# Kernel optimization log

Measured on AMD Instinct MI355X. Metric: run time of the kernel, lower is better.

## Reference

```python
import jax, jax.numpy as jnp
import numpy as np

L = 880      # flattened RootMLP param count: (1*8+8) + (8*96+96)
HID = 8      # MLP hidden width
OUT = 96     # 2*data_size
DS = 48      # data_size
T = 64       # sequence length
BATCH = 4


def setup_inputs() -> dict:
    key = jax.random.key(0)
    k1, k2, k3, k4, k5 = jax.random.split(key, 5)
    xs = jax.random.normal(k1, (BATCH, T, DS), jnp.float32)
    ts = jax.random.uniform(k2, (BATCH, T), dtype=jnp.float32)
    theta0 = 0.1 * jax.random.normal(k3, (L,), jnp.float32)
    # near-identity A so matrix powers up to A^(T-1) stay bounded
    A = 0.99 * jnp.eye(L, dtype=jnp.float32) + (0.01 / np.sqrt(L)) * jax.random.normal(k4, (L, L), jnp.float32)
    B = 0.01 * jax.random.normal(k5, (L, DS), jnp.float32)
    return {"xs": xs, "ts": ts, "theta0": theta0, "A": A, "B": B, "aux": 0}


def _forward(xs, ts, theta0, A, B):
    Bt, T_, _ = xs.shape
    I = jnp.eye(L, dtype=A.dtype)

    # A_pows[t] = A^t for t = 0..T-1, via a cumulative matmul scan
    def step(P, _):
        return P @ A, P
    _, pows = jax.lax.scan(step, I, None, length=T_)  # (T, L, L)

    # K_conv = [B, A^0(A-I)B, ..., A^(T-3)(A-I)B]  -> (T-1, L, DS)
    M = (A - I) @ B
    K_tail = jnp.einsum('tij,jd->tid', pows[:T_ - 2], M)
    K_conv = jnp.concatenate([B[None], K_tail], axis=0)

    # FFT circular convolution of input signal with K_conv over time
    u = xs[:, 1:, :]                      # (B, T-1, DS)
    u_f = jnp.fft.fft(u, axis=1)
    K_f = jnp.fft.fft(K_conv, axis=0)     # (T-1, L, DS)
    thetas = jnp.fft.ifft(jnp.einsum('tld,btd->btl', K_f, u_f), axis=1).real

    # initial-condition convolution with K_conv0 = A^tau, tau = 0..T-2
    K0 = pows[:T_ - 1]                    # (T-1, L, L)
    sig = jnp.zeros((Bt, T_ - 1, L), xs.dtype)
    sig = sig.at[:, 0, :].set(theta0)
    sig = sig.at[:, 1, :].set(-(xs[:, 0, :] @ B.T))
    sig_f = jnp.fft.fft(sig, axis=1)
    K0_f = jnp.fft.fft(K0, axis=0)
    phi0 = jnp.fft.ifft(jnp.einsum('tlm,btm->btl', K0_f, sig_f), axis=1).real

    thetas = thetas + phi0
    thetas = jnp.concatenate([jnp.broadcast_to(theta0, (Bt, 1, L)), thetas], axis=1)  # (B, T, L)

    # apply RootMLP (1 -> HID -> OUT) with params unflattened from thetas
    W0 = thetas[..., :HID]                                    # (B,T,HID): W0 is (HID,1)
    b0 = thetas[..., HID:2 * HID]
    W1 = thetas[..., 2 * HID:2 * HID + OUT * HID].reshape(Bt, T_, OUT, HID)
    b1 = thetas[..., 2 * HID + OUT * HID:]
    h = jax.nn.relu(W0 * ts[..., None] + b0)                  # (B,T,HID)
    out = jnp.einsum('btoh,bth->bto', W1, h) + b1             # (B,T,OUT)
    # reconstruction head: tanh means, softplus stds
    return jnp.concatenate([jnp.tanh(out[..., :DS]), jax.nn.softplus(out[..., DS:])], axis=-1)


def reference(xs, ts, theta0, A, B, aux):
    return _forward(xs, ts, theta0, A, B)
```

## Files before the change

### kernel.cpp

```cpp
#include <hip/hip_runtime.h>
#include <math.h>

typedef unsigned int uint;
typedef unsigned short ushort;
typedef short s16x8 __attribute__((ext_vector_type(8)));
typedef float f32x4 __attribute__((ext_vector_type(4)));
typedef uint u32x4 __attribute__((ext_vector_type(4)));

#define L     880
#define LP    896
#define NC    64
#define WSZ   (NC * LP)
#define DS    48
#define OUTD  96
#define KCV   3072
#define NZ    6

#define OFF_E    0
#define OFF_KDT  0
#define OFF_WF   4415488
#define OFF_WB   (OFF_WF + 63 * WSZ)
#define OFF_U    (OFF_WB + 63 * WSZ / 2)
#define OFF_PART (OFF_U + 256 * KCV / 2)

__device__ inline ushort f2b(float f) {
  uint u = __builtin_bit_cast(uint, f);
  u += 0x7fffu + ((u >> 16) & 1u);
  return (ushort)(u >> 16);
}
__device__ inline float b2f(ushort b) {
  uint u = ((uint)b) << 16;
  return __builtin_bit_cast(float, u);
}

__device__ __forceinline__ void gemm64(const ushort* __restrict__ Ag,
                                       const ushort* __restrict__ Bg,
                                       int Kdim, int kIters, int kOff, int m0, int n0,
                                       int tid, ushort (*As)[72], ushort (*Bs)[72],
                                       f32x4 acc[2][2]) {
  const int r = tid >> 2, kq = (tid & 3) * 16;
  const ushort* aptr = Ag + (size_t)(m0 + r) * Kdim + kOff + kq;
  const ushort* bptr = Bg + (size_t)(n0 + r) * Kdim + kOff + kq;
  const int wv = tid >> 6, lane = tid & 63;
  const int wm = (wv >> 1) * 32, wn = (wv & 1) * 32;
  const int lr = lane & 15, lg = lane >> 4;
  acc[0][0] = f32x4{0.f, 0.f, 0.f, 0.f};
  acc[0][1] = f32x4{0.f, 0.f, 0.f, 0.f};
  acc[1][0] = f32x4{0.f, 0.f, 0.f, 0.f};
  acc[1][1] = f32x4{0.f, 0.f, 0.f, 0.f};
  u32x4 ra0 = *(const u32x4*)aptr;
  u32x4 ra1 = *(const u32x4*)(aptr + 8);
  u32x4 rb0 = *(const u32x4*)bptr;
  u32x4 rb1 = *(const u32x4*)(bptr + 8);
  __syncthreads();
  *(u32x4*)&As[r][kq]     = ra0;
  *(u32x4*)&As[r][kq + 8] = ra1;
  *(u32x4*)&Bs[r][kq]     = rb0;
  *(u32x4*)&Bs[r][kq + 8] = rb1;
  if (kIters > 1) {
    ra0 = *(const u32x4*)(aptr + 64);
    ra1 = *(const u32x4*)(aptr + 72);
    rb0 = *(const u32x4*)(bptr + 64);
    rb1 = *(const u32x4*)(bptr + 72);
  }
  __syncthreads();
  for (int it = 0; it < kIters; ++it) {
    const int cur = (it & 1) * 64, nxt = cur ^ 64;
    s16x8 fa0[2], fa1[2], fb0[2], fb1[2];
#pragma unroll
    for (int k2 = 0; k2 < 2; ++k2) {
      fa0[k2] = *(const s16x8*)&As[cur + wm + lr][k2 * 32 + lg * 8];
      fa1[k2] = *(const s16x8*)&As[cur + wm + 16 + lr][k2 * 32 + lg * 8];
      fb0[k2] = *(const s16x8*)&Bs[cur + wn + lr][k2 * 32 + lg * 8];
      fb1[k2] = *(const s16x8*)&Bs[cur + wn + 16 + lr][k2 * 32 + lg * 8];
    }
    if (it + 1 < kIters) {
      *(u32x4*)&As[nxt + r][kq]     = ra0;
      *(u32x4*)&As[nxt + r][kq + 8] = ra1;
      *(u32x4*)&Bs[nxt + r][kq]     = rb0;
      *(u32x4*)&Bs[nxt + r][kq + 8] = rb1;
      if (it + 2 < kIters) {
        ra0 = *(const u32x4*)(aptr + (it + 2) * 64);
        ra1 = *(const u32x4*)(aptr + (it + 2) * 64 + 8);
        rb0 = *(const u32x4*)(bptr + (it + 2) * 64);
        rb1 = *(const u32x4*)(bptr + (it + 2) * 64 + 8);
      }
    }
#pragma unroll
    for (int k2 = 0; k2 < 2; ++k2) {
      acc[0][0] = __builtin_amdgcn_mfma_f32_16x16x32_bf16(fa0[k2], fb0[k2], acc[0][0], 0, 0, 0);
      acc[0][1] = __builtin_amdgcn_mfma_f32_16x16x32_bf16(fa0[k2], fb1[k2], acc[0][1], 0, 0, 0);
      acc[1][0] = __builtin_amdgcn_mfma_f32_16x16x32_bf16(fa1[k2], fb0[k2], acc[1][0], 0, 0, 0);
      acc[1][1] = __builtin_amdgcn_mfma_f32_16x16x32_bf16(fa1[k2], fb1[k2], acc[1][1], 0, 0, 0);
    }
    __syncthreads();
  }
}

__device__ __forceinline__ void kd_body(const float* __restrict__ WF, ushort* __restrict__ KDT,
                                        int j, int l0, int tid, float (*D)[65]) {
  __syncthreads();
  if (j < 63) {
    const float* Wj = WF + (size_t)j * WSZ;
    for (int e = tid; e < 48 * 64; e += 256) {
      int d = e >> 6, ll = e & 63;
      float v = Wj[d * LP + l0 + ll];
      if (j > 0) v -= Wj[-(int)WSZ + d * LP + l0 + ll];
      D[d][ll] = v;
    }
  } else {
    for (int e = tid; e < 48 * 64; e += 256) { int d = e >> 6, ll = e & 63; D[d][ll] = 0.f; }
  }
  __syncthreads();
  for (int e = tid; e < 48 * 64; e += 256) {
    int ll = e / 48, d = e - ll * 48;
    KDT[(size_t)(l0 + ll) * KCV + j * 48 + d] = f2b(D[d][ll]);
  }
}

__global__ __launch_bounds__(256) void k_prep(const float* __restrict__ A,
                                              const float* __restrict__ B,
                                              const float* __restrict__ th0,
                                              const float* __restrict__ xs,
                                              ushort* __restrict__ EN,
                                              ushort* __restrict__ ET,
                                              float* __restrict__ WF,
                                              ushort* __restrict__ WB,
                                              ushort* __restrict__ U) {
  const int blk = blockIdx.x;
  const int tid = threadIdx.x;
  if (blk < 196) {
    __shared__ float T[64][65];
    const int bi = (blk / 14) * 64, bj = (blk % 14) * 64;
    const int r = tid >> 2, c0 = (tid & 3) * 16;
    const int gi = bi + r;
#pragma unroll
    for (int q = 0; q < 4; ++q) {
      int c = c0 + q * 4, gj = bj + c;
      float4 v = {0.f, 0.f, 0.f, 0.f};
      if (gi < L && gj + 3 < L) {
        v = *(const float4*)(A + (size_t)gi * L + gj);
      } else if (gi < L) {
        if (gj + 0 < L) v.x = A[(size_t)gi * L + gj];
        if (gj + 1 < L) v.y = A[(size_t)gi * L + gj + 1];
        if (gj + 2 < L) v.z = A[(size_t)gi * L + gj + 2];
        if (gj + 3 < L) v.w = A[(size_t)gi * L + gj + 3];
      }
      if (gi == gj)     v.x -= 0.99f;
      if (gi == gj + 1) v.y -= 0.99f;
      if (gi == gj + 2) v.z -= 0.99f;
      if (gi == gj + 3) v.w -= 0.99f;
      T[r][c] = v.x; T[r][c + 1] = v.y; T[r][c + 2] = v.z; T[r][c + 3] = v.w;
    }
    __syncthreads();
    {
      union { ushort s[16]; u32x4 v[2]; } pk;
#pragma unroll
      for (int i = 0; i < 16; ++i) pk.s[i] = f2b(T[r][c0 + i]);
      *(u32x4*)(EN + (size_t)(bi + r) * LP + bj + c0)     = pk.v[0];
      *(u32x4*)(EN + (size_t)(bi + r) * LP + bj + c0 + 8) = pk.v[1];
    }
    {
      union { ushort s[16]; u32x4 v[2]; } pk;
#pragma unroll
      for (int i = 0; i < 16; ++i) pk.s[i] = f2b(T[c0 + i][r]);
      *(u32x4*)(ET + (size_t)(bj + r) * LP + bi + c0)     = pk.v[0];
      *(u32x4*)(ET + (size_t)(bj + r) * LP + bi + c0 + 8) = pk.v[1];
    }
  } else if (blk < 210) {
    int base = (blk - 196) * 4096;
    for (int e = tid; e < 4096; e += 256) {
      int idx = base + e;
      int c = idx / LP, l = idx % LP;
      float v = 0.f;
      if (l < L) {
        if (c < DS) v = B[l * DS + c];
        else if (c == DS) v = th0[l];
        else if (c < 53) {
          int b = c - 49;
          float s = 0.f;
          for (int d = 0; d < DS; ++d) s += B[l * DS + d] * xs[(b * 64) * DS + d];
          v = -s;
        }
      }
      WF[idx] = v;
      WB[idx] = f2b(v);
    }
  } else {
    int idx = ((blk - 210) * 256 + tid) * 4;
    int rr = idx / KCV, k = idx - rr * KCV;
    ushort4 v = {0, 0, 0, 0};
    if (rr < 252 && k < 3024) {
      int b = rr / 63, tau = rr - b * 63;
      int j = k / DS, d = k - j * DS;
      int s = tau - j; if (s < 0) s += 63;
      float4 x4 = *(const float4*)(xs + (size_t)(b * 64 + s + 1) * DS + d);
      v.x = f2b(x4.x); v.y = f2b(x4.y); v.z = f2b(x4.z); v.w = f2b(x4.w);
    }
    *(ushort4*)(U + idx) = v;
  }
}

__global__ __launch_bounds__(256) void k_ladder(
    const ushort* __restrict__ sqA, const ushort* __restrict__ sqBT, float cs2,
    ushort* __restrict__ sqOutN, ushort* __restrict__ sqOutT, int ySq,
    int nCh, const ushort* __restrict__ chWB, const ushort* __restrict__ chE, float csc,
    const float* __restrict__ chWFsrc, float* __restrict__ chWFdst,
    ushort* __restrict__ chWBdst,
    int kdJ0, const float* __restrict__ kdWF, ushort* __restrict__ kdKDT) {
  __shared__ __align__(16) ushort As[128][72];
  __shared__ __align__(16) ushort Bs[128][72];
  const int tid = threadIdx.x;
  const int y = blockIdx.y;
  const int n0 = blockIdx.x * 64;
  const int wv = tid >> 6, lane = tid & 63;
  const int wm = (wv >> 1) * 32, wn = (wv & 1) * 32;
  const int lr = lane & 15, lg = lane >> 4;

  if (y < ySq) {
    const int m0 = y * 64;
    f32x4 acc[2][2];
    gemm64(sqA, sqBT, LP, LP / 64, 0, m0, n0, tid, As, Bs, acc);
    ushort (*T)[72] = As;
#pragma unroll
    for (int fm = 0; fm < 2; ++fm)
#pragma unroll
      for (int fn = 0; fn < 2; ++fn)
#pragma unroll
        for (int rr = 0; rr < 4; ++rr) {
          int mi = wm + fm * 16 + lg * 4 + rr;
          int ni = wn + fn * 16 + lr;
          float v = acc[fm][fn][rr] + cs2 * b2f(sqA[(size_t)(m0 + mi) * LP + n0 + ni]);
          ushort bv = f2b(v);
          sqOutN[(size_t)(m0 + mi) * LP + n0 + ni] = bv;
          T[ni][mi] = bv;
        }
    if (sqOutT) {
      __syncthreads();
      const int nr = tid >> 2, ct0 = (tid & 3) * 16;
      u32x4 o0 = *(const u32x4*)&T[nr][ct0];
      u32x4 o1 = *(const u32x4*)&T[nr][ct0 + 8];
      *(u32x4*)(sqOutT + (size_t)(n0 + nr) * LP + m0 + ct0)     = o0;
      *(u32x4*)(sqOutT + (size_t)(n0 + nr) * LP + m0 + ct0 + 8) = o1;
    }
  } else if (y < ySq + nCh) {
    const int t = y - ySq;
    f32x4 acc[2][2];
    gemm64(chWB + (size_t)t * WSZ, chE, LP, LP / 64, 0, 0, n0, tid, As, Bs, acc);
    const float*  srcF = chWFsrc + (size_t)t * WSZ;
    float*        dstF = chWFdst + (size_t)t * WSZ;
    ushort*       dstB = chWBdst + (size_t)t * WSZ;
#pragma unroll
    for (int fm = 0; fm < 2; ++fm)
#pragma unroll
      for (int fn = 0; fn < 2; ++fn)
#pragma unroll
        for (int rr = 0; rr < 4; ++rr) {
          int mi = wm + fm * 16 + lg * 4 + rr;
          int ni = n0 + wn + fn * 16 + lr;
          float v = acc[fm][fn][rr] + csc * srcF[(size_t)mi * LP + ni];
          dstF[(size_t)mi * LP + ni] = v;
          dstB[(size_t)mi * LP + ni] = f2b(v);
        }
  } else {
    int j = kdJ0 + (y - ySq - nCh);
    kd_body(kdWF, kdKDT, j, n0, tid, (float(*)[65])As);
  }
}

__global__ __launch_bounds__(256) void k_kd(const float* __restrict__ WF,
                                            ushort* __restrict__ KDT, int j0) {
  __shared__ float D[48][65];
  kd_body(WF, KDT, j0 + blockIdx.y, blockIdx.x * 64, threadIdx.x, D);
}

__global__ __launch_bounds__(256) void k_conv(const ushort* __restrict__ U,
                                              const ushort* __restrict__ KDT,
                                              float* __restrict__ part) {
  __shared__ __align__(16) ushort As[128][72];
  __shared__ __align__(16) ushort Bs[128][72];
  const int tid = threadIdx.x;
  const int n0 = blockIdx.x * 64, m0 = blockIdx.y * 64;
  const int kOff = blockIdx.z * (KCV / NZ);
  const int wv = tid >> 6, lane = tid & 63;
  const int wm = (wv >> 1) * 32, wn = (wv & 1) * 32;
  const int lr = lane & 15, lg = lane >> 4;
  f32x4 acc[2][2];
  gemm64(U, KDT, KCV, (KCV / NZ) / 64, kOff, m0, n0, tid, As, Bs, acc);
  float* pp = part + (size_t)blockIdx.z * (256 * LP);
#pragma unroll
  for (int fm = 0; fm < 2; ++fm)
#pragma unroll
    for (int fn = 0; fn < 2; ++fn)
#pragma unroll
      for (int rr = 0; rr < 4; ++rr) {
        int m = m0 + wm + fm * 16 + lg * 4 + rr;
        int n = n0 + wn + fn * 16 + lr;
        pp[(size_t)m * LP + n] = acc[fm][fn][rr];
      }
}

__global__ __launch_bounds__(256) void k_final(const float* __restrict__ part,
                                               const float* __restrict__ WF,
                                               const float* __restrict__ th0,
                                               const float* __restrict__ ts,
                                               float* __restrict__ out) {
  __shared__ float th[LP];
  const int bt = blockIdx.x, b = bt >> 6, t = bt & 63;
  for (int l = threadIdx.x; l < LP; l += 256) {
    float v = 0.f;
    if (l < L) {
      if (t == 0) v = th0[l];
      else {
        int rr = b * 63 + (t - 1);
        v = 0.f;
#pragma unroll
        for (int z = 0; z < NZ; ++z) v += part[(size_t)z * (256 * LP) + rr * LP + l];
        int tau = t - 1;
        v += WF[(size_t)tau * WSZ + DS * LP + l];
        int tw = (tau + 62) % 63;
        v += WF[(size_t)tw * WSZ + (49 + b) * LP + l];
      }
    }
    th[l] = v;
  }
  __syncthreads();
  int o = threadIdx.x;
  if (o < OUTD) {
    float tv = ts[bt];
    float acc = th[784 + o];
#pragma unroll
    for (int i = 0; i < 8; ++i) {
      float h = fmaxf(th[i] * tv + th[8 + i], 0.f);
      acc += th[16 + o * 8 + i] * h;
    }
    float rs;
    if (o < DS) rs = tanhf(acc);
    else        rs = fmaxf(acc, 0.f) + log1pf(expf(-fabsf(acc)));
    out[bt * OUTD + o] = rs;
  }
}

extern "C" void kernel_launch(void* const* d_in, const int* in_sizes, int n_in,
                              void* d_out, int out_size, void* d_ws, size_t ws_size,
                              hipStream_t stream) {
  const float* xs  = (const float*)d_in[0];
  const float* ts  = (const float*)d_in[1];
  const float* th0 = (const float*)d_in[2];
  const float* A   = (const float*)d_in[3];
  const float* B   = (const float*)d_in[4];
  float* out = (float*)d_out;
  float* ws  = (float*)d_ws;

  ushort* EP   = (ushort*)(ws + OFF_E);
  const size_t PL = (size_t)LP * LP;
  ushort* EN1  = EP + 0 * PL;
  ushort* ET1  = EP + 1 * PL;
  ushort* EN2  = EP + 2 * PL;
  ushort* ET2  = EP + 3 * PL;
  ushort* EN4  = EP + 4 * PL;
  ushort* ET4  = EP + 5 * PL;
  ushort* EN8  = EP + 6 * PL;
  ushort* ET8  = EP + 7 * PL;
  ushort* EN16 = EP + 8 * PL;
  ushort* ET16 = EP + 9 * PL;
  ushort* EN32 = EP + 10 * PL;
  float*  WF   = ws + OFF_WF;
  ushort* WB   = (ushort*)(ws + OFF_WB);
  ushort* KDT  = (ushort*)(ws + OFF_KDT);
  ushort* U    = (ushort*)(ws + OFF_U);
  float*  part = ws + OFF_PART;

  const float c1 = 0.99f;
  const float c2 = c1 * c1, c4 = c2 * c2, c8 = c4 * c4, c16 = c8 * c8, c32 = c16 * c16;

  k_prep<<<978, 256, 0, stream>>>(A, B, th0, xs, EN1, ET1, WF, WB, U);

  k_ladder<<<dim3(14, 15), 256, 0, stream>>>(EN1, ET1, 2.f * c1, EN2, ET2, 14,
                                             1, WB, EN1, c1, WF, WF + 1 * WSZ, WB + (size_t)1 * WSZ,
                                             0, nullptr, nullptr);
  k_ladder<<<dim3(14, 16), 256, 0, stream>>>(EN2, ET2, 2.f * c2, EN4, ET4, 14,
                                             2, WB, EN2, c2, WF, WF + 2 * WSZ, WB + (size_t)2 * WSZ,
                                             0, nullptr, nullptr);
  k_ladder<<<dim3(14, 18), 256, 0, stream>>>(EN4, ET4, 2.f * c4, EN8, ET8, 14,
                                             4, WB, EN4, c4, WF, WF + 4 * WSZ, WB + (size_t)4 * WSZ,
                                             0, nullptr, nullptr);
  k_ladder<<<dim3(14, 22), 256, 0, stream>>>(EN8, ET8, 2.f * c8, EN16, ET16, 14,
                                             8, WB, EN8, c8, WF, WF + 8 * WSZ, WB + (size_t)8 * WSZ,
                                             0, nullptr, nullptr);
  k_ladder<<<dim3(14, 30), 256, 0, stream>>>(EN16, ET16, 2.f * c16, EN32, nullptr, 14,
                                             16, WB, EN16, c16, WF, WF + 16 * WSZ, WB + (size_t)16 * WSZ,
                                             0, nullptr, nullptr);
  k_ladder<<<dim3(14, 63), 256, 0, stream>>>(nullptr, nullptr, 0.f, nullptr, nullptr, 0,
                                             31, WB, EN32, c32, WF, WF + 32 * WSZ, WB + (size_t)32 * WSZ,
                                             0, WF, KDT);
  k_kd<<<dim3(14, 32), 256, 0, stream>>>(WF, KDT, 32);

  k_conv<<<dim3(14, 4, NZ), 256, 0, stream>>>(U, KDT, part);
  k_final<<<256, 256, 0, stream>>>(part, WF, th0, ts, out);
}
```

Baseline: 112.7 us.

## Split GEMM K-loop across two 256-thread groups with intra-block reduction

Blocks grow from 256 to 512 threads. The two halves of each block process opposite halves of the K dimension in separate LDS buffers, and partial accumulators are summed through shared memory before the epilogue. The goal is to halve the serial K-loop latency per tile in the ladder and conv GEMMs, which launch few blocks and so underfill the GPU. The cost is an extra LDS reduction and barrier, half the threads idling during the epilogue, and more LDS per block, which may limit occupancy.

```diff
diff --git a/kernel.cpp b/kernel.cpp
--- a/kernel.cpp
+++ b/kernel.cpp
@@ -23,6 +23,10 @@
 #define OFF_U    (OFF_WB + 63 * WSZ / 2)
 #define OFF_PART (OFF_U + 256 * KCV / 2)
 
+#define LROW   72
+#define LBUF   (64 * LROW)
+#define LGRP   (2 * LBUF)
+
 __device__ inline ushort f2b(float f) {
   uint u = __builtin_bit_cast(uint, f);
   u += 0x7fffu + ((u >> 16) & 1u);
@@ -33,15 +37,20 @@
   return __builtin_bit_cast(float, u);
 }
 
-__device__ __forceinline__ void gemm64(const ushort* __restrict__ Ag,
-                                       const ushort* __restrict__ Bg,
-                                       int Kdim, int kIters, int kOff, int m0, int n0,
-                                       int tid, ushort (*As)[72], ushort (*Bs)[72],
-                                       f32x4 acc[2][2]) {
-  const int r = tid >> 2, kq = (tid & 3) * 16;
-  const ushort* aptr = Ag + (size_t)(m0 + r) * Kdim + kOff + kq;
-  const ushort* bptr = Bg + (size_t)(n0 + r) * Kdim + kOff + kq;
-  const int wv = tid >> 6, lane = tid & 63;
+__device__ __forceinline__ void gemm64sk(const ushort* __restrict__ Ag,
+                                         const ushort* __restrict__ Bg,
+                                         int Kdim, int kIters, int kOff, int m0, int n0,
+                                         int tid, ushort* ldsA, ushort* ldsB,
+                                         f32x4 acc[2][2]) {
+  const int grp = tid >> 8;
+  const int t2  = tid & 255;
+  const int KH  = kIters >> 1;
+  const int gL  = grp * LGRP;
+  const int kOffG = kOff + grp * KH * 64;
+  const int r = t2 >> 2, kq = (t2 & 3) * 16;
+  const ushort* aptr = Ag + (size_t)(m0 + r) * Kdim + kOffG + kq;
+  const ushort* bptr = Bg + (size_t)(n0 + r) * Kdim + kOffG + kq;
+  const int wv = t2 >> 6, lane = tid & 63;
   const int wm = (wv >> 1) * 32, wn = (wv & 1) * 32;
   const int lr = lane & 15, lg = lane >> 4;
   acc[0][0] = f32x4{0.f, 0.f, 0.f, 0.f};
@@ -53,33 +62,34 @@
   u32x4 rb0 = *(const u32x4*)bptr;
   u32x4 rb1 = *(const u32x4*)(bptr + 8);
   __syncthreads();
-  *(u32x4*)&As[r][kq]     = ra0;
-  *(u32x4*)&As[r][kq + 8] = ra1;
-  *(u32x4*)&Bs[r][kq]     = rb0;
-  *(u32x4*)&Bs[r][kq + 8] = rb1;
-  if (kIters > 1) {
+  *(u32x4*)&ldsA[gL + r * LROW + kq]     = ra0;
+  *(u32x4*)&ldsA[gL + r * LROW + kq + 8] = ra1;
+  *(u32x4*)&ldsB[gL + r * LROW + kq]     = rb0;
+  *(u32x4*)&ldsB[gL + r * LROW + kq + 8] = rb1;
+  if (KH > 1) {
     ra0 = *(const u32x4*)(aptr + 64);
     ra1 = *(const u32x4*)(aptr + 72);
     rb0 = *(const u32x4*)(bptr + 64);
     rb1 = *(const u32x4*)(bptr + 72);
   }
   __syncthreads();
-  for (int it = 0; it < kIters; ++it) {
-    const int cur = (it & 1) * 64, nxt = cur ^ 64;
+  for (int it = 0; it < KH; ++it) {
+    const int cur = gL + (it & 1) * LBUF;
+    const int nxt = gL + ((it & 1) ^ 1) * LBUF;
     s16x8 fa0[2], fa1[2], fb0[2], fb1[2];
 #pragma unroll
     for (int k2 = 0; k2 < 2; ++k2) {
-      fa0[k2] = *(const s16x8*)&As[cur + wm + lr][k2 * 32 + lg * 8];
-      fa1[k2] = *(const s16x8*)&As[cur + wm + 16 + lr][k2 * 32 + lg * 8];
-      fb0[k2] = *(const s16x8*)&Bs[cur + wn + lr][k2 * 32 + lg * 8];
-      fb1[k2] = *(const s16x8*)&Bs[cur + wn + 16 + lr][k2 * 32 + lg * 8];
-    }
-    if (it + 1 < kIters) {
-      *(u32x4*)&As[nxt + r][kq]     = ra0;
-      *(u32x4*)&As[nxt + r][kq + 8] = ra1;
-      *(u32x4*)&Bs[nxt + r][kq]     = rb0;
-      *(u32x4*)&Bs[nxt + r][kq + 8] = rb1;
-      if (it + 2 < kIters) {
+      fa0[k2] = *(const s16x8*)&ldsA[cur + (wm + lr) * LROW + k2 * 32 + lg * 8];
+      fa1[k2] = *(const s16x8*)&ldsA[cur + (wm + 16 + lr) * LROW + k2 * 32 + lg * 8];
+      fb0[k2] = *(const s16x8*)&ldsB[cur + (wn + lr) * LROW + k2 * 32 + lg * 8];
+      fb1[k2] = *(const s16x8*)&ldsB[cur + (wn + 16 + lr) * LROW + k2 * 32 + lg * 8];
+    }
+    if (it + 1 < KH) {
+      *(u32x4*)&ldsA[nxt + r * LROW + kq]     = ra0;
+      *(u32x4*)&ldsA[nxt + r * LROW + kq + 8] = ra1;
+      *(u32x4*)&ldsB[nxt + r * LROW + kq]     = rb0;
+      *(u32x4*)&ldsB[nxt + r * LROW + kq + 8] = rb1;
+      if (it + 2 < KH) {
         ra0 = *(const u32x4*)(aptr + (it + 2) * 64);
         ra1 = *(const u32x4*)(aptr + (it + 2) * 64 + 8);
         rb0 = *(const u32x4*)(bptr + (it + 2) * 64);
@@ -95,6 +105,26 @@
     }
     __syncthreads();
   }
+  float* red = (float*)ldsA;
+  if (grp == 1) {
+#pragma unroll
+    for (int m = 0; m < 2; ++m)
+#pragma unroll
+      for (int n = 0; n < 2; ++n)
+#pragma unroll
+        for (int rr = 0; rr < 4; ++rr)
+          red[((m * 2 + n) * 4 + rr) * 256 + t2] = acc[m][n][rr];
+  }
+  __syncthreads();
+  if (grp == 0) {
+#pragma unroll
+    for (int m = 0; m < 2; ++m)
+#pragma unroll
+      for (int n = 0; n < 2; ++n)
+#pragma unroll
+        for (int rr = 0; rr < 4; ++rr)
+          acc[m][n][rr] += red[((m * 2 + n) * 4 + rr) * 256 + t2];
+  }
 }
 
 __device__ __forceinline__ void kd_body(const float* __restrict__ WF, ushort* __restrict__ KDT,
@@ -102,17 +132,17 @@
   __syncthreads();
   if (j < 63) {
     const float* Wj = WF + (size_t)j * WSZ;
-    for (int e = tid; e < 48 * 64; e += 256) {
+    for (int e = tid; e < 48 * 64; e += 512) {
       int d = e >> 6, ll = e & 63;
       float v = Wj[d * LP + l0 + ll];
       if (j > 0) v -= Wj[-(int)WSZ + d * LP + l0 + ll];
       D[d][ll] = v;
     }
   } else {
-    for (int e = tid; e < 48 * 64; e += 256) { int d = e >> 6, ll = e & 63; D[d][ll] = 0.f; }
-  }
-  __syncthreads();
-  for (int e = tid; e < 48 * 64; e += 256) {
+    for (int e = tid; e < 48 * 64; e += 512) { int d = e >> 6, ll = e & 63; D[d][ll] = 0.f; }
+  }
+  __syncthreads();
+  for (int e = tid; e < 48 * 64; e += 512) {
     int ll = e / 48, d = e - ll * 48;
     KDT[(size_t)(l0 + ll) * KCV + j * 48 + d] = f2b(D[d][ll]);
   }
@@ -201,103 +231,109 @@
   }
 }
 
-__global__ __launch_bounds__(256) void k_ladder(
+__global__ __launch_bounds__(512, 4) void k_ladder(
     const ushort* __restrict__ sqA, const ushort* __restrict__ sqBT, float cs2,
     ushort* __restrict__ sqOutN, ushort* __restrict__ sqOutT, int ySq,
     int nCh, const ushort* __restrict__ chWB, const ushort* __restrict__ chE, float csc,
     const float* __restrict__ chWFsrc, float* __restrict__ chWFdst,
     ushort* __restrict__ chWBdst,
     int kdJ0, const float* __restrict__ kdWF, ushort* __restrict__ kdKDT) {
-  __shared__ __align__(16) ushort As[128][72];
-  __shared__ __align__(16) ushort Bs[128][72];
+  __shared__ __align__(16) ushort ldsA[2 * LGRP];
+  __shared__ __align__(16) ushort ldsB[2 * LGRP];
   const int tid = threadIdx.x;
   const int y = blockIdx.y;
   const int n0 = blockIdx.x * 64;
-  const int wv = tid >> 6, lane = tid & 63;
+  const int wv = (tid & 255) >> 6, lane = tid & 63;
   const int wm = (wv >> 1) * 32, wn = (wv & 1) * 32;
   const int lr = lane & 15, lg = lane >> 4;
 
   if (y < ySq) {
     const int m0 = y * 64;
     f32x4 acc[2][2];
-    gemm64(sqA, sqBT, LP, LP / 64, 0, m0, n0, tid, As, Bs, acc);
-    ushort (*T)[72] = As;
-#pragma unroll
-    for (int fm = 0; fm < 2; ++fm)
-#pragma unroll
-      for (int fn = 0; fn < 2; ++fn)
-#pragma unroll
-        for (int rr = 0; rr < 4; ++rr) {
-          int mi = wm + fm * 16 + lg * 4 + rr;
-          int ni = wn + fn * 16 + lr;
-          float v = acc[fm][fn][rr] + cs2 * b2f(sqA[(size_t)(m0 + mi) * LP + n0 + ni]);
-          ushort bv = f2b(v);
-          sqOutN[(size_t)(m0 + mi) * LP + n0 + ni] = bv;
-          T[ni][mi] = bv;
-        }
-    if (sqOutT) {
-      __syncthreads();
+    gemm64sk(sqA, sqBT, LP, LP / 64, 0, m0, n0, tid, ldsA, ldsB, acc);
+    ushort* T = ldsB;
+    if (tid < 256) {
+#pragma unroll
+      for (int fm = 0; fm < 2; ++fm)
+#pragma unroll
+        for (int fn = 0; fn < 2; ++fn)
+#pragma unroll
+          for (int rr = 0; rr < 4; ++rr) {
+            int mi = wm + fm * 16 + lg * 4 + rr;
+            int ni = wn + fn * 16 + lr;
+            float v = acc[fm][fn][rr] + cs2 * b2f(sqA[(size_t)(m0 + mi) * LP + n0 + ni]);
+            ushort bv = f2b(v);
+            sqOutN[(size_t)(m0 + mi) * LP + n0 + ni] = bv;
+            T[ni * LROW + mi] = bv;
+          }
+    }
+    __syncthreads();
+    if (sqOutT && tid < 256) {
       const int nr = tid >> 2, ct0 = (tid & 3) * 16;
-      u32x4 o0 = *(const u32x4*)&T[nr][ct0];
-      u32x4 o1 = *(const u32x4*)&T[nr][ct0 + 8];
+      u32x4 o0 = *(const u32x4*)&T[nr * LROW + ct0];
+      u32x4 o1 = *(const u32x4*)&T[nr * LROW + ct0 + 8];
       *(u32x4*)(sqOutT + (size_t)(n0 + nr) * LP + m0 + ct0)     = o0;
       *(u32x4*)(sqOutT + (size_t)(n0 + nr) * LP + m0 + ct0 + 8) = o1;
     }
   } else if (y < ySq + nCh) {
     const int t = y - ySq;
     f32x4 acc[2][2];
-    gemm64(chWB + (size_t)t * WSZ, chE, LP, LP / 64, 0, 0, n0, tid, As, Bs, acc);
-    const float*  srcF = chWFsrc + (size_t)t * WSZ;
-    float*        dstF = chWFdst + (size_t)t * WSZ;
-    ushort*       dstB = chWBdst + (size_t)t * WSZ;
-#pragma unroll
-    for (int fm = 0; fm < 2; ++fm)
-#pragma unroll
-      for (int fn = 0; fn < 2; ++fn)
-#pragma unroll
-        for (int rr = 0; rr < 4; ++rr) {
-          int mi = wm + fm * 16 + lg * 4 + rr;
-          int ni = n0 + wn + fn * 16 + lr;
-          float v = acc[fm][fn][rr] + csc * srcF[(size_t)mi * LP + ni];
-          dstF[(size_t)mi * LP + ni] = v;
-          dstB[(size_t)mi * LP + ni] = f2b(v);
-        }
+    gemm64sk(chWB + (size_t)t * WSZ, chE, LP, LP / 64, 0, 0, n0, tid, ldsA, ldsB, acc);
+    if (tid < 256) {
+      const float*  srcF = chWFsrc + (size_t)t * WSZ;
+      float*        dstF = chWFdst + (size_t)t * WSZ;
+      ushort*       dstB = chWBdst + (size_t)t * WSZ;
+#pragma unroll
+      for (int fm = 0; fm < 2; ++fm)
+#pragma unroll
+        for (int fn = 0; fn < 2; ++fn)
+#pragma unroll
+          for (int rr = 0; rr < 4; ++rr) {
+            int mi = wm + fm * 16 + lg * 4 + rr;
+            int ni = n0 + wn + fn * 16 + lr;
+            float v = acc[fm][fn][rr] + csc * srcF[(size_t)mi * LP + ni];
+            dstF[(size_t)mi * LP + ni] = v;
+            dstB[(size_t)mi * LP + ni] = f2b(v);
+          }
+    }
   } else {
     int j = kdJ0 + (y - ySq - nCh);
-    kd_body(kdWF, kdKDT, j, n0, tid, (float(*)[65])As);
-  }
-}
-
-__global__ __launch_bounds__(256) void k_kd(const float* __restrict__ WF,
+    kd_body(kdWF, kdKDT, j, n0, tid, (float(*)[65])ldsA);
+  }
+}
+
+__global__ __launch_bounds__(512) void k_kd(const float* __restrict__ WF,
                                             ushort* __restrict__ KDT, int j0) {
   __shared__ float D[48][65];
   kd_body(WF, KDT, j0 + blockIdx.y, blockIdx.x * 64, threadIdx.x, D);
 }
 
-__global__ __launch_bounds__(256) void k_conv(const ushort* __restrict__ U,
-                                              const ushort* __restrict__ KDT,
-                                              float* __restrict__ part) {
-  __shared__ __align__(16) ushort As[128][72];
-  __shared__ __align__(16) ushort Bs[128][72];
+__global__ __launch_bounds__(512, 4) void k_conv(const ushort* __restrict__ U,
+                                                 const ushort* __restrict__ KDT,
+                                                 float* __restrict__ part) {
+  __shared__ __align__(16) ushort ldsA[2 * LGRP];
+  __shared__ __align__(16) ushort ldsB[2 * LGRP];
   const int tid = threadIdx.x;
   const int n0 = blockIdx.x * 64, m0 = blockIdx.y * 64;
   const int kOff = blockIdx.z * (KCV / NZ);
-  const int wv = tid >> 6, lane = tid & 63;
+  const int wv = (tid & 255) >> 6, lane = tid & 63;
   const int wm = (wv >> 1) * 32, wn = (wv & 1) * 32;
   const int lr = lane & 15, lg = lane >> 4;
   f32x4 acc[2][2];
-  gemm64(U, KDT, KCV, (KCV / NZ) / 64, kOff, m0, n0, tid, As, Bs, acc);
-  float* pp = part + (size_t)blockIdx.z * (256 * LP);
-#pragma unroll
-  for (int fm = 0; fm < 2; ++fm)
-#pragma unroll
-    for (int fn = 0; fn < 2; ++fn)
-#pragma unroll
-      for (int rr = 0; rr < 4; ++rr) {
-        int m = m0 + wm + fm * 16 + lg * 4 + rr;
-        int n = n0 + wn + fn * 16 + lr;
-        pp[(size_t)m * LP + n] = acc[fm][fn][rr];
-      }
+  gemm64sk(U, KDT, KCV, (KCV / NZ) / 64, kOff, m0, n0, tid, ldsA, ldsB, acc);
+  if (tid < 256) {
+    float* pp = part + (size_t)blockIdx.z * (256 * LP);
+#pragma unroll
+    for (int fm = 0; fm < 2; ++fm)
+#pragma unroll
+      for (int fn = 0; fn < 2; ++fn)
+#pragma unroll
+        for (int rr = 0; rr < 4; ++rr) {
+          int m = m0 + wm + fm * 16 + lg * 4 + rr;
+          int n = n0 + wn + fn * 16 + lr;
+          pp[(size_t)m * LP + n] = acc[fm][fn][rr];
+        }
+  }
 }
 
 __global__ __launch_bounds__(256) void k_final(const float* __restrict__ part,
@@ -376,26 +412,26 @@
 
   k_prep<<<978, 256, 0, stream>>>(A, B, th0, xs, EN1, ET1, WF, WB, U);
 
-  k_ladder<<<dim3(14, 15), 256, 0, stream>>>(EN1, ET1, 2.f * c1, EN2, ET2, 14,
+  k_ladder<<<dim3(14, 15), 512, 0, stream>>>(EN1, ET1, 2.f * c1, EN2, ET2, 14,
                                              1, WB, EN1, c1, WF, WF + 1 * WSZ, WB + (size_t)1 * WSZ,
                                              0, nullptr, nullptr);
-  k_ladder<<<dim3(14, 16), 256, 0, stream>>>(EN2, ET2, 2.f * c2, EN4, ET4, 14,
+  k_ladder<<<dim3(14, 16), 512, 0, stream>>>(EN2, ET2, 2.f * c2, EN4, ET4, 14,
                                              2, WB, EN2, c2, WF, WF + 2 * WSZ, WB + (size_t)2 * WSZ,
                                              0, nullptr, nullptr);
-  k_ladder<<<dim3(14, 18), 256, 0, stream>>>(EN4, ET4, 2.f * c4, EN8, ET8, 14,
+  k_ladder<<<dim3(14, 18), 512, 0, stream>>>(EN4, ET4, 2.f * c4, EN8, ET8, 14,
                                              4, WB, EN4, c4, WF, WF + 4 * WSZ, WB + (size_t)4 * WSZ,
                                              0, nullptr, nullptr);
-  k_ladder<<<dim3(14, 22), 256, 0, stream>>>(EN8, ET8, 2.f * c8, EN16, ET16, 14,
+  k_ladder<<<dim3(14, 22), 512, 0, stream>>>(EN8, ET8, 2.f * c8, EN16, ET16, 14,
                                              8, WB, EN8, c8, WF, WF + 8 * WSZ, WB + (size_t)8 * WSZ,
                                              0, nullptr, nullptr);
-  k_ladder<<<dim3(14, 30), 256, 0, stream>>>(EN16, ET16, 2.f * c16, EN32, nullptr, 14,
+  k_ladder<<<dim3(14, 30), 512, 0, stream>>>(EN16, ET16, 2.f * c16, EN32, nullptr, 14,
                                              16, WB, EN16, c16, WF, WF + 16 * WSZ, WB + (size_t)16 * WSZ,
                                              0, nullptr, nullptr);
-  k_ladder<<<dim3(14, 63), 256, 0, stream>>>(nullptr, nullptr, 0.f, nullptr, nullptr, 0,
+  k_ladder<<<dim3(14, 63), 512, 0, stream>>>(nullptr, nullptr, 0.f, nullptr, nullptr, 0,
                                              31, WB, EN32, c32, WF, WF + 32 * WSZ, WB + (size_t)32 * WSZ,
                                              0, WF, KDT);
-  k_kd<<<dim3(14, 32), 256, 0, stream>>>(WF, KDT, 32);
-
-  k_conv<<<dim3(14, 4, NZ), 256, 0, stream>>>(U, KDT, part);
+  k_kd<<<dim3(14, 32), 512, 0, stream>>>(WF, KDT, 32);
+
+  k_conv<<<dim3(14, 4, NZ), 512, 0, stream>>>(U, KDT, part);
   k_final<<<256, 256, 0, stream>>>(part, WF, th0, ts, out);
 }
```

Result: faster. 93.26 us (-17.3%).
